# Kernel tuning notes

Measured on AMD Instinct MI355X. Metric: run time of the kernel, lower is better.

## Reference

```python
import jax, jax.numpy as jnp
import numpy as np

B, IC, OC, K, H, W = 8, 512, 512, 3, 32, 32
GAIN, LRMUL = 1.0, 1.0
# compute_runtime_coef: fan_in = prod(weight_shape[:-1])
RC_CONV = GAIN / np.sqrt(K * K * IC) * LRMUL   # conv weight [K,K,IC,OC]
RC_DENSE = GAIN / np.sqrt(IC) * LRMUL          # dense weight [IC, IC]


def setup_inputs() -> dict:
    key = jax.random.key(0)
    ks = jax.random.split(key, 4)
    x = jax.random.normal(ks[0], (B, IC, H, W), dtype=jnp.float32)
    w = jax.random.normal(ks[1], (B, IC), dtype=jnp.float32)
    # init_std = 1/lrmul = 1.0 for both weights; bias init zeros
    conv_w = jax.random.normal(ks[2], (K, K, IC, OC), dtype=jnp.float32)
    dense_w = jax.random.normal(ks[3], (IC, IC), dtype=jnp.float32)
    dense_b = jnp.zeros((IC,), dtype=jnp.float32)
    return {"x": x, "w": w, "conv_w": conv_w, "dense_w": dense_w, "dense_b": dense_b}


def reference(x, w, conv_w, dense_w, dense_b):
    b, ic, h, wd = x.shape
    # modulation: style = Dense(w) + bias + 1
    style = w @ (RC_DENSE * dense_w) + LRMUL * dense_b + 1.0        # [B, IC]
    wt = (RC_CONV * conv_w)[None] * style[:, None, None, :, None]   # [B,K,K,IC,OC]
    # demodulation: rsqrt of sum of squares over (kh, kw, ic)
    d = jax.lax.rsqrt(jnp.sum(jnp.square(wt), axis=(1, 2, 3)) + 1e-8)  # [B, OC]
    wt = wt * d[:, None, None, None, :]
    # grouped conv with groups = batch: weight -> OIHW [B*OC, IC, K, K]
    w_g = jnp.transpose(wt, (0, 4, 3, 1, 2)).reshape(b * OC, ic, K, K)
    xg = x.reshape(1, b * ic, h, wd)
    y = jax.lax.conv_general_dilated(
        xg, w_g, window_strides=(1, 1), padding="SAME",
        dimension_numbers=("NCHW", "OIHW", "NCHW"), feature_group_count=b)
    return y.reshape(b, OC, h, wd)
```

## Files before the change

### kernel.cpp

```cpp
#include <hip/hip_runtime.h>
#include <stdint.h>


#define B_   8
#define IC_  512
#define OC_  512

static constexpr float RC_DENSE = 0.04419417382415922f;
static constexpr float RC_CONV  = 0.014731391274719739f;

typedef _Float16 half8    __attribute__((ext_vector_type(8)));
typedef float    floatx16 __attribute__((ext_vector_type(16)));

__device__ __forceinline__ void g2l(const void* g, void* l) {
  __builtin_amdgcn_global_load_lds(
      (const __attribute__((address_space(1))) void*)g,
      (__attribute__((address_space(3))) void*)l, 16, 0, 0);
}

__global__ __launch_bounds__(256) void wts_kernel(
    const float* __restrict__ cw, _Float16* __restrict__ Wtf,
    float* __restrict__ S) {
  const int by = blockIdx.x, icb = blockIdx.y;
  const int oc0 = by * 64, ic0 = icb * 32;
  const int oc = threadIdx.x & 63, g = threadIdx.x >> 6;
  __shared__ _Float16 LA[18432];
  float sq[8] = {};
  for (int m = 0; m < 72; ++m) {
    int r = g + 4 * m;
    int t = r >> 5, icl = r & 31;
    float v = cw[(size_t)(t * IC_ + ic0 + icl) * OC_ + oc0 + oc];
    sq[m & 7] += v * v;
    int kk = (icl >> 4) & 1, kq2 = (icl >> 3) & 1, j = icl & 7;
    LA[(((t * 2 + kk) * 2 + kq2) * 64 + oc) * 8 + j] = (_Float16)v;
  }
  for (int s2 = 0; s2 < 8; ++s2)
    S[(size_t)(ic0 + g + 4 * s2) * OC_ + oc0 + oc] = sq[s2];
  __syncthreads();
  _Float16* dst = Wtf + (size_t)(by * 16 + icb) * 18432;
  for (int i = 0; i < 9; ++i) {
    int c = i * 256 + threadIdx.x;
    *(half8*)(dst + (size_t)c * 8) = *(const half8*)&LA[c * 8];
  }
}

__global__ __launch_bounds__(256) void style_kernel(
    const float* __restrict__ wv, const float* __restrict__ dw,
    const float* __restrict__ db, float* __restrict__ sm,
    float* __restrict__ sm2) {
  const int b = blockIdx.y;
  const int i = blockIdx.x * 64 + (threadIdx.x & 63);
  const int jg = threadIdx.x >> 6;
  __shared__ float red[4][64];
  float p = 0.f;
  for (int j = jg * 128; j < jg * 128 + 128; ++j)
    p += wv[b * IC_ + j] * dw[(size_t)j * IC_ + i];
  red[jg][threadIdx.x & 63] = p;
  __syncthreads();
  if (threadIdx.x < 64) {
    float s = red[0][threadIdx.x] + red[1][threadIdx.x] +
              red[2][threadIdx.x] + red[3][threadIdx.x];
    s = s * RC_DENSE + db[i] + 1.0f;
    float v = s * RC_CONV;
    sm[b * IC_ + i] = v;
    sm2[b * IC_ + i] = v * v;
  }
}

__global__ __launch_bounds__(256) void d_kernel(
    const float* __restrict__ S, const float* __restrict__ sm2,
    float* __restrict__ dvec) {
  const int b = blockIdx.y;
  const int oc = blockIdx.x * 64 + (threadIdx.x & 63);
  const int g = threadIdx.x >> 6;
  __shared__ float red[4][64];
  float p = 0.f;
  for (int ic = g * 128; ic < g * 128 + 128; ++ic)
    p += sm2[b * IC_ + ic] * S[(size_t)ic * OC_ + oc];
  red[g][threadIdx.x & 63] = p;
  __syncthreads();
  if (threadIdx.x < 64) {
    float s = red[0][threadIdx.x] + red[1][threadIdx.x] +
              red[2][threadIdx.x] + red[3][threadIdx.x];
    dvec[b * OC_ + oc] = rsqrtf(s + 1e-8f);
  }
}

__global__ __launch_bounds__(256) void xsp_kernel(
    const float* __restrict__ x, const float* __restrict__ sm,
    _Float16* __restrict__ xsp) {
  const int h = blockIdx.x, b = blockIdx.y;
  __shared__ _Float16 Xt[32 * 520];
  const int tid = threadIdx.x;
  for (int k = 0; k < 16; ++k) {
    int idx = k * 256 + tid;
    int ic = idx >> 3, wc = (idx & 7) * 4;
    float4 v = *(const float4*)&x[((size_t)(b * IC_ + ic) * 32 + h) * 32 + wc];
    float s = sm[b * IC_ + ic];
    Xt[(wc + 0) * 520 + ic] = (_Float16)(v.x * s);
    Xt[(wc + 1) * 520 + ic] = (_Float16)(v.y * s);
    Xt[(wc + 2) * 520 + ic] = (_Float16)(v.z * s);
    Xt[(wc + 3) * 520 + ic] = (_Float16)(v.w * s);
  }
  __syncthreads();
  _Float16* xb = xsp + (size_t)b * 16 * 36992;
  const int r = h + 1;
  half8 z = {};
  for (int it = 0; it < 9; ++it) {
    int c = it * 256 + tid;
    if (c < 2176) {
      int icb = c / 136, rem = c - 136 * icb, kkq = rem / 34, C = rem - 34 * kkq;
      half8 val = z;
      if (C != 0 && C != 33)
        val = *(const half8*)&Xt[(C - 1) * 520 + icb * 32 + kkq * 8];
      *(half8*)&xb[(size_t)icb * 36992 + (size_t)r * 1088 + kkq * 272 + C * 8] = val;
    }
  }
  if (h == 0 || h == 31) {
    const int rz = (h == 0) ? 0 : 33;
    for (int it = 0; it < 9; ++it) {
      int c = it * 256 + tid;
      if (c < 2176) {
        int icb = c / 136, rem = c - 136 * icb, kkq = rem / 34, C = rem - 34 * kkq;
        *(half8*)&xb[(size_t)icb * 36992 + (size_t)rz * 1088 + kkq * 272 + C * 8] = z;
      }
    }
  }
}

__global__ __launch_bounds__(256) void conv_kernel(
    const _Float16* __restrict__ Wtf,
    const _Float16* __restrict__ xsp,
    const float* __restrict__ dvec,
    float* __restrict__ out) {
  const int bx = blockIdx.x, by = blockIdx.y, b = blockIdx.z;
  const int tid = threadIdx.x, lane = tid & 63, w = tid >> 6;
  const int wm = w & 1, wn = w >> 1;
  const int n = lane & 31, kq = lane >> 5;
  const int h0 = bx * 8;

  __shared__ _Float16 Xb[2][10880];

  const _Float16* gX = xsp + (size_t)b * 16 * 36992 + (size_t)h0 * 1088;
  const _Float16* gA = Wtf + (size_t)(by * 16) * 18432;
  const int aoff = kq * 512 + (wm * 32 + n) * 8;

  for (int i = 0; i < 6; ++i) {
    int c = i * 256 + tid;
    if (c < 1360) g2l(gX + (size_t)c * 8, &Xb[0][c * 8]);
  }
  half8 a[9][2], an[9][2];
#pragma unroll
  for (int t = 0; t < 9; ++t)
#pragma unroll
    for (int kk = 0; kk < 2; ++kk)
      a[t][kk] = *(const half8*)(gA + aoff + (t * 2 + kk) * 1024);

  floatx16 acc[4] = {};
  int cur = 0;
  for (int icb = 0; icb < 16; ++icb) {
    __syncthreads();
    if (icb < 15) {
      const _Float16* gA1 = gA + (size_t)(icb + 1) * 18432 + aoff;
#pragma unroll
      for (int t = 0; t < 9; ++t)
#pragma unroll
        for (int kk = 0; kk < 2; ++kk)
          an[t][kk] = *(const half8*)(gA1 + (t * 2 + kk) * 1024);
      const _Float16* gX1 = gX + (size_t)(icb + 1) * 36992;
      for (int i = 0; i < 6; ++i) {
        int c = i * 256 + tid;
        if (c < 1360) g2l(gX1 + (size_t)c * 8, &Xb[cur ^ 1][c * 8]);
      }
    }
    const _Float16* Xp = &Xb[cur][0] + (wn * 4) * 1088 + kq * 272 + n * 8;
#pragma unroll
    for (int rr = 0; rr < 6; ++rr) {
#pragma unroll
      for (int kw = 0; kw < 3; ++kw) {
#pragma unroll
        for (int kk = 0; kk < 2; ++kk) {
          half8 xv = *(const half8*)(Xp + rr * 1088 + kk * 544 + kw * 8);
#pragma unroll
          for (int kh = 0; kh < 3; ++kh) {
            int pr = rr - kh;
            if (pr >= 0 && pr < 4)
              acc[pr] = __builtin_amdgcn_mfma_f32_32x32x16_f16(
                  a[kh * 3 + kw][kk], xv, acc[pr], 0, 0, 0);
          }
        }
      }
    }
#pragma unroll
    for (int t = 0; t < 9; ++t) { a[t][0] = an[t][0]; a[t][1] = an[t][1]; }
    cur ^= 1;
  }

  const int oc0 = by * 64 + wm * 32;
  const int r0 = h0 + wn * 4;
#pragma unroll
  for (int rg = 0; rg < 16; ++rg) {
    const int row = (rg & 3) + 8 * (rg >> 2) + 4 * kq;
    const float dv = dvec[b * OC_ + oc0 + row];
    float* op = out + ((size_t)b * OC_ + oc0 + row) * 1024 + r0 * 32 + n;
#pragma unroll
    for (int pr = 0; pr < 4; ++pr)
      op[pr * 32] = acc[pr][rg] * dv;
  }
}

extern "C" void kernel_launch(void* const* d_in, const int* in_sizes, int n_in,
                              void* d_out, int out_size, void* d_ws, size_t ws_size,
                              hipStream_t stream) {
  const float* x       = (const float*)d_in[0];
  const float* w       = (const float*)d_in[1];
  const float* conv_w  = (const float*)d_in[2];
  const float* dense_w = (const float*)d_in[3];
  const float* dense_b = (const float*)d_in[4];
  float* out = (float*)d_out;

  char* ws = (char*)d_ws;
  float*    sm   = (float*)ws;
  float*    sm2  = (float*)(ws + (16 << 10));
  float*    dvec = (float*)(ws + (32 << 10));
  float*    S    = (float*)(ws + (48 << 10));
  _Float16* Wtf  = (_Float16*)(ws + (48 << 10) + (1 << 20));
  _Float16* xsp  = (_Float16*)(ws + (48 << 10) + (1 << 20) + 4718592);

  wts_kernel<<<dim3(8, 16), 256, 0, stream>>>(conv_w, Wtf, S);
  style_kernel<<<dim3(8, B_), 256, 0, stream>>>(w, dense_w, dense_b, sm, sm2);
  xsp_kernel<<<dim3(32, B_), 256, 0, stream>>>(x, sm, xsp);
  d_kernel<<<dim3(8, B_), 256, 0, stream>>>(S, sm2, dvec);
  conv_kernel<<<dim3(4, 8, B_), 256, 0, stream>>>(Wtf, xsp, dvec, out);
}
```

Measured before the change: 151.2 us.

## Fuse demodulation into weight prep with atomics and halve conv row tile

Removes the separate d_kernel and the S buffer. wts_kernel now runs after style_kernel and atomically accumulates the sm2-weighted squared sums into dacc, with rsqrt applied in the conv epilogue. The conv kernel tile shrinks from 8 to 4 output rows per block, which doubles the grid to 512 blocks and asks for 2 blocks per CU. It also stops prefetching weights into registers and loads the A fragments inside each ic-block iteration instead. The aims are to cut launch overhead and improve occupancy, at the cost of exposed global weight-load latency, more total weight traffic, and atomics that make dacc summation order nondeterministic.

Result: slower. 189.2 us (+25.1%).

```diff
diff --git a/kernel.cpp b/kernel.cpp
--- a/kernel.cpp
+++ b/kernel.cpp
@@ -18,36 +18,10 @@
       (__attribute__((address_space(3))) void*)l, 16, 0, 0);
 }
 
-__global__ __launch_bounds__(256) void wts_kernel(
-    const float* __restrict__ cw, _Float16* __restrict__ Wtf,
-    float* __restrict__ S) {
-  const int by = blockIdx.x, icb = blockIdx.y;
-  const int oc0 = by * 64, ic0 = icb * 32;
-  const int oc = threadIdx.x & 63, g = threadIdx.x >> 6;
-  __shared__ _Float16 LA[18432];
-  float sq[8] = {};
-  for (int m = 0; m < 72; ++m) {
-    int r = g + 4 * m;
-    int t = r >> 5, icl = r & 31;
-    float v = cw[(size_t)(t * IC_ + ic0 + icl) * OC_ + oc0 + oc];
-    sq[m & 7] += v * v;
-    int kk = (icl >> 4) & 1, kq2 = (icl >> 3) & 1, j = icl & 7;
-    LA[(((t * 2 + kk) * 2 + kq2) * 64 + oc) * 8 + j] = (_Float16)v;
-  }
-  for (int s2 = 0; s2 < 8; ++s2)
-    S[(size_t)(ic0 + g + 4 * s2) * OC_ + oc0 + oc] = sq[s2];
-  __syncthreads();
-  _Float16* dst = Wtf + (size_t)(by * 16 + icb) * 18432;
-  for (int i = 0; i < 9; ++i) {
-    int c = i * 256 + threadIdx.x;
-    *(half8*)(dst + (size_t)c * 8) = *(const half8*)&LA[c * 8];
-  }
-}
-
 __global__ __launch_bounds__(256) void style_kernel(
     const float* __restrict__ wv, const float* __restrict__ dw,
     const float* __restrict__ db, float* __restrict__ sm,
-    float* __restrict__ sm2) {
+    float* __restrict__ sm2, float* __restrict__ dacc) {
   const int b = blockIdx.y;
   const int i = blockIdx.x * 64 + (threadIdx.x & 63);
   const int jg = threadIdx.x >> 6;
@@ -64,25 +38,43 @@
     float v = s * RC_CONV;
     sm[b * IC_ + i] = v;
     sm2[b * IC_ + i] = v * v;
-  }
-}
-
-__global__ __launch_bounds__(256) void d_kernel(
-    const float* __restrict__ S, const float* __restrict__ sm2,
-    float* __restrict__ dvec) {
-  const int b = blockIdx.y;
-  const int oc = blockIdx.x * 64 + (threadIdx.x & 63);
-  const int g = threadIdx.x >> 6;
+    dacc[b * IC_ + i] = 0.f;
+  }
+}
+
+__global__ __launch_bounds__(256) void wts_kernel(
+    const float* __restrict__ cw, const float* __restrict__ sm2,
+    _Float16* __restrict__ Wtf, float* __restrict__ dacc) {
+  const int by = blockIdx.x, icb = blockIdx.y;
+  const int oc0 = by * 64, ic0 = icb * 32;
+  const int oc = threadIdx.x & 63, g = threadIdx.x >> 6;
+  __shared__ _Float16 LA[18432];
   __shared__ float red[4][64];
-  float p = 0.f;
-  for (int ic = g * 128; ic < g * 128 + 128; ++ic)
-    p += sm2[b * IC_ + ic] * S[(size_t)ic * OC_ + oc];
-  red[g][threadIdx.x & 63] = p;
+  float sq[8] = {};
+  for (int m = 0; m < 72; ++m) {
+    int r = g + 4 * m;
+    int t = r >> 5, icl = r & 31;
+    float v = cw[(size_t)(t * IC_ + ic0 + icl) * OC_ + oc0 + oc];
+    sq[m & 7] += v * v;
+    int kk = (icl >> 4) & 1, kq2 = (icl >> 3) & 1, j = icl & 7;
+    LA[(((t * 2 + kk) * 2 + kq2) * 64 + oc) * 8 + j] = (_Float16)v;
+  }
   __syncthreads();
-  if (threadIdx.x < 64) {
-    float s = red[0][threadIdx.x] + red[1][threadIdx.x] +
-              red[2][threadIdx.x] + red[3][threadIdx.x];
-    dvec[b * OC_ + oc] = rsqrtf(s + 1e-8f);
+  _Float16* dst = Wtf + (size_t)(by * 16 + icb) * 18432;
+  for (int i = 0; i < 9; ++i) {
+    int c = i * 256 + threadIdx.x;
+    *(half8*)(dst + (size_t)c * 8) = *(const half8*)&LA[c * 8];
+  }
+  for (int b = 0; b < 8; ++b) {
+    float p = 0.f;
+    for (int s2 = 0; s2 < 8; ++s2)
+      p += sm2[b * IC_ + ic0 + g + 4 * s2] * sq[s2];
+    red[g][oc] = p;
+    __syncthreads();
+    if (g == 0)
+      atomicAdd(&dacc[b * OC_ + oc0 + oc],
+                red[0][oc] + red[1][oc] + red[2][oc] + red[3][oc]);
+    __syncthreads();
   }
 }
 
@@ -128,84 +120,75 @@
   }
 }
 
-__global__ __launch_bounds__(256) void conv_kernel(
+__global__ __launch_bounds__(256, 2) void conv_kernel(
     const _Float16* __restrict__ Wtf,
     const _Float16* __restrict__ xsp,
-    const float* __restrict__ dvec,
+    const float* __restrict__ dacc,
     float* __restrict__ out) {
   const int bx = blockIdx.x, by = blockIdx.y, b = blockIdx.z;
   const int tid = threadIdx.x, lane = tid & 63, w = tid >> 6;
   const int wm = w & 1, wn = w >> 1;
   const int n = lane & 31, kq = lane >> 5;
-  const int h0 = bx * 8;
-
-  __shared__ _Float16 Xb[2][10880];
+  const int h0 = bx * 4;
+
+  __shared__ _Float16 Xb[2][6528];
 
   const _Float16* gX = xsp + (size_t)b * 16 * 36992 + (size_t)h0 * 1088;
   const _Float16* gA = Wtf + (size_t)(by * 16) * 18432;
   const int aoff = kq * 512 + (wm * 32 + n) * 8;
 
-  for (int i = 0; i < 6; ++i) {
+  for (int i = 0; i < 4; ++i) {
     int c = i * 256 + tid;
-    if (c < 1360) g2l(gX + (size_t)c * 8, &Xb[0][c * 8]);
-  }
-  half8 a[9][2], an[9][2];
-#pragma unroll
-  for (int t = 0; t < 9; ++t)
-#pragma unroll
-    for (int kk = 0; kk < 2; ++kk)
-      a[t][kk] = *(const half8*)(gA + aoff + (t * 2 + kk) * 1024);
-
-  floatx16 acc[4] = {};
-  int cur = 0;
+    if (c < 816) g2l(gX + (size_t)c * 8, &Xb[0][c * 8]);
+  }
+
+  floatx16 acc[2] = {};
   for (int icb = 0; icb < 16; ++icb) {
+    const int cur = icb & 1;
     __syncthreads();
     if (icb < 15) {
-      const _Float16* gA1 = gA + (size_t)(icb + 1) * 18432 + aoff;
-#pragma unroll
-      for (int t = 0; t < 9; ++t)
-#pragma unroll
-        for (int kk = 0; kk < 2; ++kk)
-          an[t][kk] = *(const half8*)(gA1 + (t * 2 + kk) * 1024);
       const _Float16* gX1 = gX + (size_t)(icb + 1) * 36992;
-      for (int i = 0; i < 6; ++i) {
+      for (int i = 0; i < 4; ++i) {
         int c = i * 256 + tid;
-        if (c < 1360) g2l(gX1 + (size_t)c * 8, &Xb[cur ^ 1][c * 8]);
+        if (c < 816) g2l(gX1 + (size_t)c * 8, &Xb[cur ^ 1][c * 8]);
       }
     }
-    const _Float16* Xp = &Xb[cur][0] + (wn * 4) * 1088 + kq * 272 + n * 8;
-#pragma unroll
-    for (int rr = 0; rr < 6; ++rr) {
+    const _Float16* gAi = gA + (size_t)icb * 18432 + aoff;
+    half8 a[9][2];
+#pragma unroll
+    for (int t = 0; t < 9; ++t)
+#pragma unroll
+      for (int kk = 0; kk < 2; ++kk)
+        a[t][kk] = *(const half8*)(gAi + (t * 2 + kk) * 1024);
+    const _Float16* Xp = &Xb[cur][0] + (wn * 2) * 1088 + kq * 272 + n * 8;
+#pragma unroll
+    for (int s = 0; s < 4; ++s) {
 #pragma unroll
       for (int kw = 0; kw < 3; ++kw) {
 #pragma unroll
         for (int kk = 0; kk < 2; ++kk) {
-          half8 xv = *(const half8*)(Xp + rr * 1088 + kk * 544 + kw * 8);
+          half8 xv = *(const half8*)(Xp + s * 1088 + kk * 544 + kw * 8);
 #pragma unroll
           for (int kh = 0; kh < 3; ++kh) {
-            int pr = rr - kh;
-            if (pr >= 0 && pr < 4)
-              acc[pr] = __builtin_amdgcn_mfma_f32_32x32x16_f16(
-                  a[kh * 3 + kw][kk], xv, acc[pr], 0, 0, 0);
+            int j = s - kh;
+            if (j >= 0 && j < 2)
+              acc[j] = __builtin_amdgcn_mfma_f32_32x32x16_f16(
+                  a[kh * 3 + kw][kk], xv, acc[j], 0, 0, 0);
           }
         }
       }
     }
-#pragma unroll
-    for (int t = 0; t < 9; ++t) { a[t][0] = an[t][0]; a[t][1] = an[t][1]; }
-    cur ^= 1;
   }
 
   const int oc0 = by * 64 + wm * 32;
-  const int r0 = h0 + wn * 4;
+  const int r0 = h0 + wn * 2;
 #pragma unroll
   for (int rg = 0; rg < 16; ++rg) {
     const int row = (rg & 3) + 8 * (rg >> 2) + 4 * kq;
-    const float dv = dvec[b * OC_ + oc0 + row];
+    const float dv = rsqrtf(dacc[b * OC_ + oc0 + row] + 1e-8f);
     float* op = out + ((size_t)b * OC_ + oc0 + row) * 1024 + r0 * 32 + n;
-#pragma unroll
-    for (int pr = 0; pr < 4; ++pr)
-      op[pr * 32] = acc[pr][rg] * dv;
+    op[0]  = acc[0][rg] * dv;
+    op[32] = acc[1][rg] * dv;
   }
 }
 
@@ -222,14 +205,12 @@
   char* ws = (char*)d_ws;
   float*    sm   = (float*)ws;
   float*    sm2  = (float*)(ws + (16 << 10));
-  float*    dvec = (float*)(ws + (32 << 10));
-  float*    S    = (float*)(ws + (48 << 10));
-  _Float16* Wtf  = (_Float16*)(ws + (48 << 10) + (1 << 20));
-  _Float16* xsp  = (_Float16*)(ws + (48 << 10) + (1 << 20) + 4718592);
-
-  wts_kernel<<<dim3(8, 16), 256, 0, stream>>>(conv_w, Wtf, S);
-  style_kernel<<<dim3(8, B_), 256, 0, stream>>>(w, dense_w, dense_b, sm, sm2);
+  float*    dacc = (float*)(ws + (32 << 10));
+  _Float16* Wtf  = (_Float16*)(ws + (48 << 10));
+  _Float16* xsp  = (_Float16*)(ws + (48 << 10) + 4718592);
+
+  style_kernel<<<dim3(8, B_), 256, 0, stream>>>(w, dense_w, dense_b, sm, sm2, dacc);
+  wts_kernel<<<dim3(8, 16), 256, 0, stream>>>(conv_w, sm2, Wtf, dacc);
   xsp_kernel<<<dim3(32, B_), 256, 0, stream>>>(x, sm, xsp);
-  d_kernel<<<dim3(8, B_), 256, 0, stream>>>(S, sm2, dvec);
-  conv_kernel<<<dim3(4, 8, B_), 256, 0, stream>>>(Wtf, xsp, dvec, out);
-}
+  conv_kernel<<<dim3(8, 8, B_), 256, 0, stream>>>(Wtf, xsp, dacc, out);
+}
```

## Fuse prep kernels, fold demod reduction into weight prep, split-K conv with atomics

Applied to the files above, without the earlier changes.

Merges the weight-transform, demodulation and input-prep kernels into one launch. The weight blocks now compute the per-batch demod sums directly with atomicAdd, so the S matrix and d_kernel are gone. The conv is split over two halves of the input channels to double the grid (512 blocks instead of 256), and each half accumulates into the output with float atomics. This needs a memset of the output and adds atomic write traffic on 16 MB of output.

Measured after the change: 151.7 us. Within noise of the previous version (+0.3%).

```diff
diff --git a/kernel.cpp b/kernel.cpp
--- a/kernel.cpp
+++ b/kernel.cpp
@@ -18,36 +18,10 @@
       (__attribute__((address_space(3))) void*)l, 16, 0, 0);
 }
 
-__global__ __launch_bounds__(256) void wts_kernel(
-    const float* __restrict__ cw, _Float16* __restrict__ Wtf,
-    float* __restrict__ S) {
-  const int by = blockIdx.x, icb = blockIdx.y;
-  const int oc0 = by * 64, ic0 = icb * 32;
-  const int oc = threadIdx.x & 63, g = threadIdx.x >> 6;
-  __shared__ _Float16 LA[18432];
-  float sq[8] = {};
-  for (int m = 0; m < 72; ++m) {
-    int r = g + 4 * m;
-    int t = r >> 5, icl = r & 31;
-    float v = cw[(size_t)(t * IC_ + ic0 + icl) * OC_ + oc0 + oc];
-    sq[m & 7] += v * v;
-    int kk = (icl >> 4) & 1, kq2 = (icl >> 3) & 1, j = icl & 7;
-    LA[(((t * 2 + kk) * 2 + kq2) * 64 + oc) * 8 + j] = (_Float16)v;
-  }
-  for (int s2 = 0; s2 < 8; ++s2)
-    S[(size_t)(ic0 + g + 4 * s2) * OC_ + oc0 + oc] = sq[s2];
-  __syncthreads();
-  _Float16* dst = Wtf + (size_t)(by * 16 + icb) * 18432;
-  for (int i = 0; i < 9; ++i) {
-    int c = i * 256 + threadIdx.x;
-    *(half8*)(dst + (size_t)c * 8) = *(const half8*)&LA[c * 8];
-  }
-}
-
 __global__ __launch_bounds__(256) void style_kernel(
     const float* __restrict__ wv, const float* __restrict__ dw,
     const float* __restrict__ db, float* __restrict__ sm,
-    float* __restrict__ sm2) {
+    float* __restrict__ sm2, float* __restrict__ dacc) {
   const int b = blockIdx.y;
   const int i = blockIdx.x * 64 + (threadIdx.x & 63);
   const int jg = threadIdx.x >> 6;
@@ -64,65 +38,88 @@
     float v = s * RC_CONV;
     sm[b * IC_ + i] = v;
     sm2[b * IC_ + i] = v * v;
-  }
-}
-
-__global__ __launch_bounds__(256) void d_kernel(
-    const float* __restrict__ S, const float* __restrict__ sm2,
-    float* __restrict__ dvec) {
-  const int b = blockIdx.y;
-  const int oc = blockIdx.x * 64 + (threadIdx.x & 63);
-  const int g = threadIdx.x >> 6;
-  __shared__ float red[4][64];
-  float p = 0.f;
-  for (int ic = g * 128; ic < g * 128 + 128; ++ic)
-    p += sm2[b * IC_ + ic] * S[(size_t)ic * OC_ + oc];
-  red[g][threadIdx.x & 63] = p;
-  __syncthreads();
-  if (threadIdx.x < 64) {
-    float s = red[0][threadIdx.x] + red[1][threadIdx.x] +
-              red[2][threadIdx.x] + red[3][threadIdx.x];
-    dvec[b * OC_ + oc] = rsqrtf(s + 1e-8f);
-  }
-}
-
-__global__ __launch_bounds__(256) void xsp_kernel(
+    dacc[b * IC_ + i] = 0.f;
+  }
+}
+
+__global__ __launch_bounds__(256) void prep_kernel(
+    const float* __restrict__ cw, const float* __restrict__ sm2,
     const float* __restrict__ x, const float* __restrict__ sm,
+    _Float16* __restrict__ Wtf, float* __restrict__ dacc,
     _Float16* __restrict__ xsp) {
-  const int h = blockIdx.x, b = blockIdx.y;
-  __shared__ _Float16 Xt[32 * 520];
+  __shared__ __align__(16) char smem[45056];
+  const int bid = blockIdx.x;
   const int tid = threadIdx.x;
-  for (int k = 0; k < 16; ++k) {
-    int idx = k * 256 + tid;
-    int ic = idx >> 3, wc = (idx & 7) * 4;
-    float4 v = *(const float4*)&x[((size_t)(b * IC_ + ic) * 32 + h) * 32 + wc];
-    float s = sm[b * IC_ + ic];
-    Xt[(wc + 0) * 520 + ic] = (_Float16)(v.x * s);
-    Xt[(wc + 1) * 520 + ic] = (_Float16)(v.y * s);
-    Xt[(wc + 2) * 520 + ic] = (_Float16)(v.z * s);
-    Xt[(wc + 3) * 520 + ic] = (_Float16)(v.w * s);
-  }
-  __syncthreads();
-  _Float16* xb = xsp + (size_t)b * 16 * 36992;
-  const int r = h + 1;
-  half8 z = {};
-  for (int it = 0; it < 9; ++it) {
-    int c = it * 256 + tid;
-    if (c < 2176) {
-      int icb = c / 136, rem = c - 136 * icb, kkq = rem / 34, C = rem - 34 * kkq;
-      half8 val = z;
-      if (C != 0 && C != 33)
-        val = *(const half8*)&Xt[(C - 1) * 520 + icb * 32 + kkq * 8];
-      *(half8*)&xb[(size_t)icb * 36992 + (size_t)r * 1088 + kkq * 272 + C * 8] = val;
-    }
-  }
-  if (h == 0 || h == 31) {
-    const int rz = (h == 0) ? 0 : 33;
+  if (bid < 128) {
+    _Float16* LA = (_Float16*)smem;
+    float* redall = (float*)(smem + 36864);
+    const int by = bid >> 4, icb = bid & 15;
+    const int oc0 = by * 64, ic0 = icb * 32;
+    const int oc = tid & 63, g = tid >> 6;
+    float sq[8] = {};
+    for (int m = 0; m < 72; ++m) {
+      int r = g + 4 * m;
+      int t = r >> 5, icl = r & 31;
+      float v = cw[(size_t)(t * IC_ + ic0 + icl) * OC_ + oc0 + oc];
+      sq[m & 7] += v * v;
+      int kk = (icl >> 4) & 1, kq2 = (icl >> 3) & 1, j = icl & 7;
+      LA[(((t * 2 + kk) * 2 + kq2) * 64 + oc) * 8 + j] = (_Float16)v;
+    }
+    for (int b = 0; b < 8; ++b) {
+      float p = 0.f;
+      for (int s2 = 0; s2 < 8; ++s2)
+        p += sm2[b * IC_ + ic0 + g + 4 * s2] * sq[s2];
+      redall[(b * 4 + g) * 64 + oc] = p;
+    }
+    __syncthreads();
+    _Float16* dst = Wtf + (size_t)(by * 16 + icb) * 18432;
+    for (int i = 0; i < 9; ++i) {
+      int c = i * 256 + tid;
+      *(half8*)(dst + (size_t)c * 8) = *(const half8*)&LA[c * 8];
+    }
+    const int bb = tid >> 6;
+    for (int h = 0; h < 2; ++h) {
+      int b = bb + h * 4;
+      float s = redall[(b * 4 + 0) * 64 + oc] + redall[(b * 4 + 1) * 64 + oc] +
+                redall[(b * 4 + 2) * 64 + oc] + redall[(b * 4 + 3) * 64 + oc];
+      atomicAdd(&dacc[b * OC_ + oc0 + oc], s);
+    }
+  } else {
+    _Float16* Xt = (_Float16*)smem;
+    const int r2 = bid - 128;
+    const int h = r2 >> 3, b = r2 & 7;
+    for (int k = 0; k < 16; ++k) {
+      int idx = k * 256 + tid;
+      int ic = idx >> 3, wc = (idx & 7) * 4;
+      float4 v = *(const float4*)&x[((size_t)(b * IC_ + ic) * 32 + h) * 32 + wc];
+      float s = sm[b * IC_ + ic];
+      Xt[(wc + 0) * 520 + ic] = (_Float16)(v.x * s);
+      Xt[(wc + 1) * 520 + ic] = (_Float16)(v.y * s);
+      Xt[(wc + 2) * 520 + ic] = (_Float16)(v.z * s);
+      Xt[(wc + 3) * 520 + ic] = (_Float16)(v.w * s);
+    }
+    __syncthreads();
+    _Float16* xb = xsp + (size_t)b * 16 * 36992;
+    const int r = h + 1;
+    half8 z = {};
     for (int it = 0; it < 9; ++it) {
       int c = it * 256 + tid;
       if (c < 2176) {
         int icb = c / 136, rem = c - 136 * icb, kkq = rem / 34, C = rem - 34 * kkq;
-        *(half8*)&xb[(size_t)icb * 36992 + (size_t)rz * 1088 + kkq * 272 + C * 8] = z;
+        half8 val = z;
+        if (C != 0 && C != 33)
+          val = *(const half8*)&Xt[(C - 1) * 520 + icb * 32 + kkq * 8];
+        *(half8*)&xb[(size_t)icb * 36992 + (size_t)r * 1088 + kkq * 272 + C * 8] = val;
+      }
+    }
+    if (h == 0 || h == 31) {
+      const int rz = (h == 0) ? 0 : 33;
+      for (int it = 0; it < 9; ++it) {
+        int c = it * 256 + tid;
+        if (c < 2176) {
+          int icb = c / 136, rem = c - 136 * icb, kkq = rem / 34, C = rem - 34 * kkq;
+          *(half8*)&xb[(size_t)icb * 36992 + (size_t)rz * 1088 + kkq * 272 + C * 8] = z;
+        }
       }
     }
   }
@@ -131,9 +128,10 @@
 __global__ __launch_bounds__(256) void conv_kernel(
     const _Float16* __restrict__ Wtf,
     const _Float16* __restrict__ xsp,
-    const float* __restrict__ dvec,
+    const float* __restrict__ dacc,
     float* __restrict__ out) {
-  const int bx = blockIdx.x, by = blockIdx.y, b = blockIdx.z;
+  const int bx = blockIdx.x, by = blockIdx.y;
+  const int b = blockIdx.z >> 1, ks = blockIdx.z & 1;
   const int tid = threadIdx.x, lane = tid & 63, w = tid >> 6;
   const int wm = w & 1, wn = w >> 1;
   const int n = lane & 31, kq = lane >> 5;
@@ -141,8 +139,8 @@
 
   __shared__ _Float16 Xb[2][10880];
 
-  const _Float16* gX = xsp + (size_t)b * 16 * 36992 + (size_t)h0 * 1088;
-  const _Float16* gA = Wtf + (size_t)(by * 16) * 18432;
+  const _Float16* gX = xsp + ((size_t)b * 16 + ks * 8) * 36992 + (size_t)h0 * 1088;
+  const _Float16* gA = Wtf + (size_t)(by * 16 + ks * 8) * 18432;
   const int aoff = kq * 512 + (wm * 32 + n) * 8;
 
   for (int i = 0; i < 6; ++i) {
@@ -157,10 +155,10 @@
       a[t][kk] = *(const half8*)(gA + aoff + (t * 2 + kk) * 1024);
 
   floatx16 acc[4] = {};
-  int cur = 0;
-  for (int icb = 0; icb < 16; ++icb) {
+  for (int icb = 0; icb < 8; ++icb) {
+    const int cur = icb & 1;
     __syncthreads();
-    if (icb < 15) {
+    if (icb < 7) {
       const _Float16* gA1 = gA + (size_t)(icb + 1) * 18432 + aoff;
 #pragma unroll
       for (int t = 0; t < 9; ++t)
@@ -193,7 +191,6 @@
     }
 #pragma unroll
     for (int t = 0; t < 9; ++t) { a[t][0] = an[t][0]; a[t][1] = an[t][1]; }
-    cur ^= 1;
   }
 
   const int oc0 = by * 64 + wm * 32;
@@ -201,11 +198,11 @@
 #pragma unroll
   for (int rg = 0; rg < 16; ++rg) {
     const int row = (rg & 3) + 8 * (rg >> 2) + 4 * kq;
-    const float dv = dvec[b * OC_ + oc0 + row];
+    const float dv = rsqrtf(dacc[b * OC_ + oc0 + row] + 1e-8f);
     float* op = out + ((size_t)b * OC_ + oc0 + row) * 1024 + r0 * 32 + n;
 #pragma unroll
     for (int pr = 0; pr < 4; ++pr)
-      op[pr * 32] = acc[pr][rg] * dv;
+      atomicAdd(&op[pr * 32], acc[pr][rg] * dv);
   }
 }
 
@@ -222,14 +219,12 @@
   char* ws = (char*)d_ws;
   float*    sm   = (float*)ws;
   float*    sm2  = (float*)(ws + (16 << 10));
-  float*    dvec = (float*)(ws + (32 << 10));
-  float*    S    = (float*)(ws + (48 << 10));
-  _Float16* Wtf  = (_Float16*)(ws + (48 << 10) + (1 << 20));
-  _Float16* xsp  = (_Float16*)(ws + (48 << 10) + (1 << 20) + 4718592);
-
-  wts_kernel<<<dim3(8, 16), 256, 0, stream>>>(conv_w, Wtf, S);
-  style_kernel<<<dim3(8, B_), 256, 0, stream>>>(w, dense_w, dense_b, sm, sm2);
-  xsp_kernel<<<dim3(32, B_), 256, 0, stream>>>(x, sm, xsp);
-  d_kernel<<<dim3(8, B_), 256, 0, stream>>>(S, sm2, dvec);
-  conv_kernel<<<dim3(4, 8, B_), 256, 0, stream>>>(Wtf, xsp, dvec, out);
-}
+  float*    dacc = (float*)(ws + (32 << 10));
+  _Float16* Wtf  = (_Float16*)(ws + (48 << 10));
+  _Float16* xsp  = (_Float16*)(ws + (48 << 10) + 4718592);
+
+  hipMemsetAsync(out, 0, (size_t)B_ * OC_ * 1024 * sizeof(float), stream);
+  style_kernel<<<dim3(8, B_), 256, 0, stream>>>(w, dense_w, dense_b, sm, sm2, dacc);
+  prep_kernel<<<384, 256, 0, stream>>>(conv_w, sm2, x, sm, Wtf, dacc, xsp);
+  conv_kernel<<<dim3(4, 8, 16), 256, 0, stream>>>(Wtf, xsp, dacc, out);
+}
```
